# Kernel tuning notes

Measured on AMD Instinct MI355X. Metric: run time of the kernel, lower is better.

## Reference

```python
import jax, jax.numpy as jnp
import numpy as np


def _box_filter(x, k):
    """Mean filter with border-count normalization (count_include_pad=False).
    x: [B, C, H, W] float. Returns same shape.
    """
    B, C, H, W = x.shape
    pad = (k - 1) // 2
    ones_k = jnp.ones((1, 1, k, k), dtype=x.dtype)
    # Sum over kxk window with zero padding: treat channels as batch.
    xs = x.reshape(B * C, 1, H, W)
    win_sum = jax.lax.conv_general_dilated(
        xs, ones_k, window_strides=(1, 1), padding=[(pad, pad), (pad, pad)],
        dimension_numbers=("NCHW", "OIHW", "NCHW"))
    win_sum = win_sum.reshape(B, C, H, W)
    # Count of valid (in-bounds) taps per output pixel; independent of B, C.
    ones_img = jnp.ones((1, 1, H, W), dtype=x.dtype)
    counts = jax.lax.conv_general_dilated(
        ones_img, ones_k, window_strides=(1, 1), padding=[(pad, pad), (pad, pad)],
        dimension_numbers=("NCHW", "OIHW", "NCHW"))  # [1,1,H,W]
    return win_sum / counts


def setup_inputs() -> dict:
    key = jax.random.key(0)
    x = jax.random.normal(key, (32, 3, 512, 512), dtype=jnp.float32)
    return {"x": x, "k_size": 5}


def reference(x, k_size):
    return _box_filter(x, k_size)
```

## Files before the change

### kernel.cpp

```cpp
#include <hip/hip_runtime.h>


#define HH 512
#define WW 512
#define NPLANES 96
#define SROWS 32
#define STRIPS (HH / SROWS)

__global__ __launch_bounds__(64, 4) void box5_kernel(const float* __restrict__ x,
                                                     float* __restrict__ out) {
    const int lane = threadIdx.x;
    const int gid = blockIdx.x;
    const int plane = gid / STRIPS;
    const int strip = gid % STRIPS;
    const int y0 = strip * SROWS;
    const int ylast = y0 + SROWS + 1;

    const float* px = x + (size_t)plane * (HH * WW);
    float* pout = out + (size_t)plane * (HH * WW);

    const int w0 = lane * 8;

    float inv_cw[8];
#pragma unroll
    for (int j = 0; j < 8; ++j) {
        int w = w0 + j;
        int cw = min(w + 2, WW - 1) - max(w - 2, 0) + 1;
        inv_cw[j] = 1.0f / (float)cw;
    }

    float h[5][8];
#pragma unroll
    for (int r = 0; r < 5; ++r)
#pragma unroll
        for (int j = 0; j < 8; ++j) h[r][j] = 0.0f;

    auto rowptr = [&](int y) {
        int yc = min(max(y, 0), HH - 1);
        return px + (size_t)yc * WW + w0;
    };

    float4 a0, b0, a1, b1;
    {
        const float* p = rowptr(y0 - 2);
        a0 = *(const float4*)(p);
        b0 = *(const float4*)(p + 4);
        p = rowptr(y0 - 1);
        a1 = *(const float4*)(p);
        b1 = *(const float4*)(p + 4);
    }

    for (int y_in = y0 - 2; y_in <= ylast; ++y_in) {
        float4 a2, b2;
        {
            int yp = y_in + 2;
            if (yp > ylast) yp = ylast;
            const float* p = rowptr(yp);
            a2 = *(const float4*)(p);
            b2 = *(const float4*)(p + 4);
        }

        float xv0 = a0.x, xv1 = a0.y, xv2 = a0.z, xv3 = a0.w;
        float xv4 = b0.x, xv5 = b0.y, xv6 = b0.z, xv7 = b0.w;

        float xm2 = __shfl_up(xv6, 1);
        float xm1 = __shfl_up(xv7, 1);
        float xp1 = __shfl_down(xv0, 1);
        float xp2 = __shfl_down(xv1, 1);
        if (lane == 0)  { xm2 = 0.0f; xm1 = 0.0f; }
        if (lane == 63) { xp1 = 0.0f; xp2 = 0.0f; }

        const float mask = (y_in >= 0 && y_in < HH) ? 1.0f : 0.0f;

        float hn[8];
        float t = xm2 + xm1 + xv0 + xv1 + xv2;
        hn[0] = t;
        t += xv3 - xm2; hn[1] = t;
        t += xv4 - xm1; hn[2] = t;
        t += xv5 - xv0; hn[3] = t;
        t += xv6 - xv1; hn[4] = t;
        t += xv7 - xv2; hn[5] = t;
        t += xp1 - xv3; hn[6] = t;
        t += xp2 - xv4; hn[7] = t;
#pragma unroll
        for (int j = 0; j < 8; ++j) hn[j] *= mask;

#pragma unroll
        for (int r = 0; r < 4; ++r)
#pragma unroll
            for (int j = 0; j < 8; ++j) h[r][j] = h[r + 1][j];
#pragma unroll
        for (int j = 0; j < 8; ++j) h[4][j] = hn[j];

        const int y_out = y_in - 2;
        if (y_out >= y0 && y_out < y0 + SROWS) {
            int ch = min(y_out + 2, HH - 1) - max(y_out - 2, 0) + 1;
            float inv_ch = 1.0f / (float)ch;
            float o[8];
#pragma unroll
            for (int j = 0; j < 8; ++j) {
                float vs = h[0][j] + h[1][j] + h[2][j] + h[3][j] + h[4][j];
                o[j] = vs * (inv_cw[j] * inv_ch);
            }
            float* po = pout + (size_t)y_out * WW + w0;
            *(float4*)(po)     = make_float4(o[0], o[1], o[2], o[3]);
            *(float4*)(po + 4) = make_float4(o[4], o[5], o[6], o[7]);
        }

        a0 = a1; b0 = b1; a1 = a2; b1 = b2;
    }
}

extern "C" void kernel_launch(void* const* d_in, const int* in_sizes, int n_in,
                              void* d_out, int out_size, void* d_ws, size_t ws_size,
                              hipStream_t stream) {
    const float* x = (const float*)d_in[0];
    float* out = (float*)d_out;
    dim3 grid(NPLANES * STRIPS);
    box5_kernel<<<grid, 64, 0, stream>>>(x, out);
}
```

Before: 185.7 us.

## Load all strip rows up front into registers with smaller strips

Each block now handles 8 output rows instead of 32 and issues all 12 input row loads at once into registers, then computes the horizontal sums and writes the outputs in fully unrolled loops. This replaces the serial one-row-ahead prefetch loop, which exposed memory latency on every step, with a single burst of independent loads, and the grid grows fourfold. In exchange, redundant halo reads rise from 4 of 36 rows to 4 of 12 rows per strip, and register pressure goes up (launch bounds lowered to 2).

```diff
diff --git a/kernel.cpp b/kernel.cpp
--- a/kernel.cpp
+++ b/kernel.cpp
@@ -4,22 +4,60 @@
 #define HH 512
 #define WW 512
 #define NPLANES 96
-#define SROWS 32
+#define SROWS 8
 #define STRIPS (HH / SROWS)
+#define NROWS (SROWS + 4)
 
-__global__ __launch_bounds__(64, 4) void box5_kernel(const float* __restrict__ x,
+__global__ __launch_bounds__(64, 2) void box5_kernel(const float* __restrict__ x,
                                                      float* __restrict__ out) {
     const int lane = threadIdx.x;
     const int gid = blockIdx.x;
     const int plane = gid / STRIPS;
     const int strip = gid % STRIPS;
     const int y0 = strip * SROWS;
-    const int ylast = y0 + SROWS + 1;
 
     const float* px = x + (size_t)plane * (HH * WW);
     float* pout = out + (size_t)plane * (HH * WW);
+    const int w0 = lane * 8;
 
-    const int w0 = lane * 8;
+    float4 ra[NROWS], rb[NROWS];
+#pragma unroll
+    for (int r = 0; r < NROWS; ++r) {
+        int y = y0 - 2 + r;
+        int yc = min(max(y, 0), HH - 1);
+        const float* p = px + (size_t)yc * WW + w0;
+        ra[r] = *(const float4*)(p);
+        rb[r] = *(const float4*)(p + 4);
+    }
+
+    float hs[NROWS][8];
+#pragma unroll
+    for (int r = 0; r < NROWS; ++r) {
+        const int y = y0 - 2 + r;
+        const float mask = (y >= 0 && y < HH) ? 1.0f : 0.0f;
+
+        const float xv0 = ra[r].x, xv1 = ra[r].y, xv2 = ra[r].z, xv3 = ra[r].w;
+        const float xv4 = rb[r].x, xv5 = rb[r].y, xv6 = rb[r].z, xv7 = rb[r].w;
+
+        float xm2 = __shfl_up(xv6, 1);
+        float xm1 = __shfl_up(xv7, 1);
+        float xp1 = __shfl_down(xv0, 1);
+        float xp2 = __shfl_down(xv1, 1);
+        if (lane == 0)  { xm2 = 0.0f; xm1 = 0.0f; }
+        if (lane == 63) { xp1 = 0.0f; xp2 = 0.0f; }
+
+        float t = xm2 + xm1 + xv0 + xv1 + xv2;
+        hs[r][0] = t;
+        t += xv3 - xm2; hs[r][1] = t;
+        t += xv4 - xm1; hs[r][2] = t;
+        t += xv5 - xv0; hs[r][3] = t;
+        t += xv6 - xv1; hs[r][4] = t;
+        t += xv7 - xv2; hs[r][5] = t;
+        t += xp1 - xv3; hs[r][6] = t;
+        t += xp2 - xv4; hs[r][7] = t;
+#pragma unroll
+        for (int j = 0; j < 8; ++j) hs[r][j] *= mask;
+    }
 
     float inv_cw[8];
 #pragma unroll
@@ -29,85 +67,21 @@
         inv_cw[j] = 1.0f / (float)cw;
     }
 
-    float h[5][8];
 #pragma unroll
-    for (int r = 0; r < 5; ++r)
+    for (int o = 0; o < SROWS; ++o) {
+        const int y_out = y0 + o;
+        const int ch = min(y_out + 2, HH - 1) - max(y_out - 2, 0) + 1;
+        const float inv_ch = 1.0f / (float)ch;
+
+        float ov[8];
 #pragma unroll
-        for (int j = 0; j < 8; ++j) h[r][j] = 0.0f;
-
-    auto rowptr = [&](int y) {
-        int yc = min(max(y, 0), HH - 1);
-        return px + (size_t)yc * WW + w0;
-    };
-
-    float4 a0, b0, a1, b1;
-    {
-        const float* p = rowptr(y0 - 2);
-        a0 = *(const float4*)(p);
-        b0 = *(const float4*)(p + 4);
-        p = rowptr(y0 - 1);
-        a1 = *(const float4*)(p);
-        b1 = *(const float4*)(p + 4);
-    }
-
-    for (int y_in = y0 - 2; y_in <= ylast; ++y_in) {
-        float4 a2, b2;
-        {
-            int yp = y_in + 2;
-            if (yp > ylast) yp = ylast;
-            const float* p = rowptr(yp);
-            a2 = *(const float4*)(p);
-            b2 = *(const float4*)(p + 4);
+        for (int j = 0; j < 8; ++j) {
+            float vs = hs[o][j] + hs[o + 1][j] + hs[o + 2][j] + hs[o + 3][j] + hs[o + 4][j];
+            ov[j] = vs * (inv_cw[j] * inv_ch);
         }
-
-        float xv0 = a0.x, xv1 = a0.y, xv2 = a0.z, xv3 = a0.w;
-        float xv4 = b0.x, xv5 = b0.y, xv6 = b0.z, xv7 = b0.w;
-
-        float xm2 = __shfl_up(xv6, 1);
-        float xm1 = __shfl_up(xv7, 1);
-        float xp1 = __shfl_down(xv0, 1);
-        float xp2 = __shfl_down(xv1, 1);
-        if (lane == 0)  { xm2 = 0.0f; xm1 = 0.0f; }
-        if (lane == 63) { xp1 = 0.0f; xp2 = 0.0f; }
-
-        const float mask = (y_in >= 0 && y_in < HH) ? 1.0f : 0.0f;
-
-        float hn[8];
-        float t = xm2 + xm1 + xv0 + xv1 + xv2;
-        hn[0] = t;
-        t += xv3 - xm2; hn[1] = t;
-        t += xv4 - xm1; hn[2] = t;
-        t += xv5 - xv0; hn[3] = t;
-        t += xv6 - xv1; hn[4] = t;
-        t += xv7 - xv2; hn[5] = t;
-        t += xp1 - xv3; hn[6] = t;
-        t += xp2 - xv4; hn[7] = t;
-#pragma unroll
-        for (int j = 0; j < 8; ++j) hn[j] *= mask;
-
-#pragma unroll
-        for (int r = 0; r < 4; ++r)
-#pragma unroll
-            for (int j = 0; j < 8; ++j) h[r][j] = h[r + 1][j];
-#pragma unroll
-        for (int j = 0; j < 8; ++j) h[4][j] = hn[j];
-
-        const int y_out = y_in - 2;
-        if (y_out >= y0 && y_out < y0 + SROWS) {
-            int ch = min(y_out + 2, HH - 1) - max(y_out - 2, 0) + 1;
-            float inv_ch = 1.0f / (float)ch;
-            float o[8];
-#pragma unroll
-            for (int j = 0; j < 8; ++j) {
-                float vs = h[0][j] + h[1][j] + h[2][j] + h[3][j] + h[4][j];
-                o[j] = vs * (inv_cw[j] * inv_ch);
-            }
-            float* po = pout + (size_t)y_out * WW + w0;
-            *(float4*)(po)     = make_float4(o[0], o[1], o[2], o[3]);
-            *(float4*)(po + 4) = make_float4(o[4], o[5], o[6], o[7]);
-        }
-
-        a0 = a1; b0 = b1; a1 = a2; b1 = b2;
+        float* po = pout + (size_t)y_out * WW + w0;
+        *(float4*)(po)     = make_float4(ov[0], ov[1], ov[2], ov[3]);
+        *(float4*)(po + 4) = make_float4(ov[4], ov[5], ov[6], ov[7]);
     }
 }
 
```

Result: no change. 187.1 us (+0.8%).
